# Performance work log

Measured on AMD Instinct MI355X. Metric: run time of the kernel, lower is better.

The kernel has to match this reference:

```python
import jax, jax.numpy as jnp
import numpy as np

N_NODES = 50000
N_EDGES = 800000
NUM_FEATURES = 256
HIDDEN = 256
EMBED = 128


def gcn_conv(x, edge_index, W, b, n_nodes):
    """PyG GCNConv: add self-loops, symmetric normalization, linear (no bias),
    scatter-add aggregation to destination nodes, then add bias."""
    loop = jnp.arange(n_nodes, dtype=edge_index.dtype)
    src = jnp.concatenate([edge_index[0], loop])  # [E + N]
    dst = jnp.concatenate([edge_index[1], loop])  # [E + N]
    # degree of destination nodes (edge weight = 1, self-loop weight = 1)
    deg = jax.ops.segment_sum(jnp.ones_like(src, dtype=x.dtype), dst,
                              num_segments=n_nodes)
    dis = jnp.where(deg > 0, jax.lax.rsqrt(jnp.maximum(deg, 1.0)), 0.0)
    norm = dis[src] * dis[dst]  # [E + N]
    xw = x @ W  # [N, out] project first (cheaper gather when out <= in)
    msg = xw[src] * norm[:, None]  # [E + N, out]
    out = jax.ops.segment_sum(msg, dst, num_segments=n_nodes)
    return out + b


def setup_inputs() -> dict:
    key = jax.random.key(0)
    k1, k2, k3, k4 = jax.random.split(key, 4)
    x = jax.random.normal(k1, (N_NODES, NUM_FEATURES), dtype=jnp.float32)
    edge_index = jax.random.randint(k2, (2, N_EDGES), 0, N_NODES, dtype=jnp.int32)
    W1 = jax.random.normal(k3, (NUM_FEATURES, HIDDEN), dtype=jnp.float32) / np.sqrt(NUM_FEATURES)
    b1 = jnp.zeros((HIDDEN,), dtype=jnp.float32)
    W2 = jax.random.normal(k4, (HIDDEN, EMBED), dtype=jnp.float32) / np.sqrt(HIDDEN)
    b2 = jnp.zeros((EMBED,), dtype=jnp.float32)
    return {"x": x, "edge_index": edge_index, "W1": W1, "b1": b1, "W2": W2, "b2": b2}


def reference(x, edge_index, W1, b1, W2, b2):
    n = x.shape[0]
    h = jax.nn.relu(gcn_conv(x, edge_index, W1, b1, n))
    return gcn_conv(h, edge_index, W2, b2, n)
```

## Files before the change

### kernel.cpp

```cpp
#include <hip/hip_runtime.h>
#include <hip/hip_bf16.h>

#define K_DIM 256

typedef __attribute__((ext_vector_type(8))) short short8;
typedef __attribute__((ext_vector_type(4))) float f32x4;


__global__ void degree_hist_kernel(const int* __restrict__ dst, int E,
                                   int* __restrict__ cnt) {
    int e = blockIdx.x * blockDim.x + threadIdx.x;
    if (e < E) atomicAdd(&cnt[dst[e]], 1);
}

constexpr int SCAN_C = 512;

__global__ __launch_bounds__(256) void scan_phase1(const int* __restrict__ cnt,
                                                   int* __restrict__ bsum, int N) {
    const int t = threadIdx.x;
    const int i0 = blockIdx.x * SCAN_C + 2 * t;
    int s = 0;
    if (i0 < N) s += cnt[i0];
    if (i0 + 1 < N) s += cnt[i0 + 1];
    __shared__ int sh[256];
    sh[t] = s;
    __syncthreads();
    for (int off = 128; off > 0; off >>= 1) {
        if (t < off) sh[t] += sh[t + off];
        __syncthreads();
    }
    if (t == 0) bsum[blockIdx.x] = sh[0];
}

__global__ __launch_bounds__(256) void scan_phase2(int* __restrict__ bsum, int nb,
                                                   int* __restrict__ row_ptr, int N) {
    const int t = threadIdx.x;
    int v = (t < nb) ? bsum[t] : 0;
    __shared__ int sh[256];
    sh[t] = v;
    __syncthreads();
    for (int off = 1; off < 256; off <<= 1) {
        int u = (t >= off) ? sh[t - off] : 0;
        __syncthreads();
        sh[t] += u;
        __syncthreads();
    }
    if (t < nb) bsum[t] = (t == 0) ? 0 : sh[t - 1];
    if (t == 255) row_ptr[N] = sh[255];
}

__global__ __launch_bounds__(256) void scan_phase3(const int* __restrict__ cnt,
                                                   const int* __restrict__ bsum,
                                                   int* __restrict__ row_ptr,
                                                   int* __restrict__ fill,
                                                   float* __restrict__ dis, int N) {
    const int t = threadIdx.x;
    const int i0 = blockIdx.x * SCAN_C + 2 * t;
    const int c0 = (i0 < N) ? cnt[i0] : 0;
    const int c1 = (i0 + 1 < N) ? cnt[i0 + 1] : 0;
    __shared__ int sh[256];
    sh[t] = c0 + c1;
    __syncthreads();
    for (int off = 1; off < 256; off <<= 1) {
        int u = (t >= off) ? sh[t - off] : 0;
        __syncthreads();
        sh[t] += u;
        __syncthreads();
    }
    const int excl = ((t == 0) ? 0 : sh[t - 1]) + bsum[blockIdx.x];
    if (i0 < N) {
        row_ptr[i0] = excl;
        fill[i0] = excl;
        dis[i0] = rsqrtf((float)(c0 + 1));
    }
    if (i0 + 1 < N) {
        row_ptr[i0 + 1] = excl + c0;
        fill[i0 + 1] = excl + c0;
        dis[i0 + 1] = rsqrtf((float)(c1 + 1));
    }
}

__global__ void build_csr_kernel(const int* __restrict__ src,
                                 const int* __restrict__ dst, int E,
                                 int* __restrict__ fill, int* __restrict__ col,
                                 const float* __restrict__ dis,
                                 float* __restrict__ wnorm) {
    int e = blockIdx.x * blockDim.x + threadIdx.x;
    if (e < E) {
        int s = src[e];
        int d = dst[e];
        int pos = atomicAdd(&fill[d], 1);
        col[pos] = s;
        wnorm[pos] = dis[s] * dis[d];
    }
}


__device__ __forceinline__ unsigned short bf16_hi(float v) {
    __hip_bfloat16 h = __float2bfloat16(v);
    return *(unsigned short*)&h;
}
__device__ __forceinline__ float bf16_back(unsigned short u) {
    __hip_bfloat16 h = *(__hip_bfloat16*)&u;
    return __bfloat162float(h);
}
__device__ __forceinline__ float bf2f(unsigned short u) {
    unsigned int b = ((unsigned int)u) << 16;
    float f;
    __builtin_memcpy(&f, &b, 4);
    return f;
}


template <int NCOLS>
__global__ __launch_bounds__(256) void gemm_mfma_kernel(const float* __restrict__ A,
                                                        const float* __restrict__ B,
                                                        unsigned short* __restrict__ C,
                                                        int M) {
    __shared__ unsigned short As_hi[128][40];
    __shared__ unsigned short As_lo[128][40];
    __shared__ unsigned short Bs_hi[128][40];
    __shared__ unsigned short Bs_lo[128][40];

    const int t = threadIdx.x;
    const int lane = t & 63;
    const int wid = t >> 6;
    const int wm = wid >> 1;
    const int wn = wid & 1;
    const int m0 = blockIdx.y * 128;
    const int n0 = blockIdx.x * 128;

    f32x4 acc[4][4];
#pragma unroll
    for (int i = 0; i < 4; ++i)
#pragma unroll
        for (int j = 0; j < 4; ++j) acc[i][j] = (f32x4)(0.f);

    const int a_r = t >> 3;
    const int a_c4 = t & 7;
    const int b_col = t & 127;
    const int b_kq0 = t >> 7;

    for (int k0 = 0; k0 < K_DIM; k0 += 32) {
        __syncthreads();

#pragma unroll
        for (int p = 0; p < 4; ++p) {
            const int row = a_r + p * 32;
            const int grow = min(m0 + row, M - 1);
            const float4 v = *(const float4*)(A + (size_t)grow * K_DIM + k0 + a_c4 * 4);
            unsigned short h0 = bf16_hi(v.x), h1 = bf16_hi(v.y),
                           h2 = bf16_hi(v.z), h3 = bf16_hi(v.w);
            unsigned short l0 = bf16_hi(v.x - bf16_back(h0)),
                           l1 = bf16_hi(v.y - bf16_back(h1)),
                           l2 = bf16_hi(v.z - bf16_back(h2)),
                           l3 = bf16_hi(v.w - bf16_back(h3));
            *(ushort4*)&As_hi[row][a_c4 * 4] = make_ushort4(h0, h1, h2, h3);
            *(ushort4*)&As_lo[row][a_c4 * 4] = make_ushort4(l0, l1, l2, l3);
        }

#pragma unroll
        for (int p = 0; p < 4; ++p) {
            const int kq = b_kq0 + p * 2;
            float v0 = B[(size_t)(k0 + kq * 4 + 0) * NCOLS + n0 + b_col];
            float v1 = B[(size_t)(k0 + kq * 4 + 1) * NCOLS + n0 + b_col];
            float v2 = B[(size_t)(k0 + kq * 4 + 2) * NCOLS + n0 + b_col];
            float v3 = B[(size_t)(k0 + kq * 4 + 3) * NCOLS + n0 + b_col];
            unsigned short h0 = bf16_hi(v0), h1 = bf16_hi(v1),
                           h2 = bf16_hi(v2), h3 = bf16_hi(v3);
            unsigned short l0 = bf16_hi(v0 - bf16_back(h0)),
                           l1 = bf16_hi(v1 - bf16_back(h1)),
                           l2 = bf16_hi(v2 - bf16_back(h2)),
                           l3 = bf16_hi(v3 - bf16_back(h3));
            *(ushort4*)&Bs_hi[b_col][kq * 4] = make_ushort4(h0, h1, h2, h3);
            *(ushort4*)&Bs_lo[b_col][kq * 4] = make_ushort4(l0, l1, l2, l3);
        }

        __syncthreads();

        const int fr = lane & 15;
        const int fk = (lane >> 4) * 8;
        short8 a_hi[4], a_lo[4], b_hi[4], b_lo[4];
#pragma unroll
        for (int fm = 0; fm < 4; ++fm) {
            const int r = wm * 64 + fm * 16 + fr;
            a_hi[fm] = *(const short8*)&As_hi[r][fk];
            a_lo[fm] = *(const short8*)&As_lo[r][fk];
        }
#pragma unroll
        for (int fn = 0; fn < 4; ++fn) {
            const int c = wn * 64 + fn * 16 + fr;
            b_hi[fn] = *(const short8*)&Bs_hi[c][fk];
            b_lo[fn] = *(const short8*)&Bs_lo[c][fk];
        }

#pragma unroll
        for (int fm = 0; fm < 4; ++fm)
#pragma unroll
            for (int fn = 0; fn < 4; ++fn) {
                acc[fm][fn] = __builtin_amdgcn_mfma_f32_16x16x32_bf16(
                    a_hi[fm], b_hi[fn], acc[fm][fn], 0, 0, 0);
                acc[fm][fn] = __builtin_amdgcn_mfma_f32_16x16x32_bf16(
                    a_hi[fm], b_lo[fn], acc[fm][fn], 0, 0, 0);
                acc[fm][fn] = __builtin_amdgcn_mfma_f32_16x16x32_bf16(
                    a_lo[fm], b_hi[fn], acc[fm][fn], 0, 0, 0);
            }
    }

    const int c_col = n0 + wn * 64 + (lane & 15);
    const int r_base = m0 + wm * 64 + (lane >> 4) * 4;
#pragma unroll
    for (int fm = 0; fm < 4; ++fm)
#pragma unroll
        for (int fn = 0; fn < 4; ++fn)
#pragma unroll
            for (int r = 0; r < 4; ++r) {
                const int row = r_base + fm * 16 + r;
                if (row < M)
                    C[(size_t)row * NCOLS + c_col + fn * 16] = bf16_hi(acc[fm][fn][r]);
            }
}


template <int F, bool RELU>
__global__ __launch_bounds__(256) void aggregate_kernel(
    const unsigned short* __restrict__ xw, const int* __restrict__ row_ptr,
    const int* __restrict__ col, const float* __restrict__ wnorm,
    const float* __restrict__ dis, const float* __restrict__ bias,
    float* __restrict__ out, int N) {
    constexpr int VEC = F / 64;
    const int wid = threadIdx.x >> 6;
    const int lane = threadIdx.x & 63;
    const int n = blockIdx.x * 4 + wid;
    if (n >= N) return;

    const float dn = dis[n];
    float acc[VEC];
    {
        const float w = dn * dn;
        const unsigned short* xn = xw + (size_t)n * F + lane * VEC;
        if (VEC == 4) {
            const ushort4 u = *(const ushort4*)xn;
            acc[0] = bf2f(u.x) * w;
            acc[1] = bf2f(u.y) * w;
            acc[2] = bf2f(u.z) * w;
            acc[3] = bf2f(u.w) * w;
        } else {
            const ushort2 u = *(const ushort2*)xn;
            acc[0] = bf2f(u.x) * w;
            acc[1] = bf2f(u.y) * w;
        }
    }

    const int e0 = row_ptr[n];
    const int e1 = row_ptr[n + 1];
    int e = e0;
    for (; e + 2 <= e1; e += 2) {
        const int s0 = col[e];
        const int s1 = col[e + 1];
        const float w0 = wnorm[e];
        const float w1 = wnorm[e + 1];
        const unsigned short* x0 = xw + (size_t)s0 * F + lane * VEC;
        const unsigned short* x1 = xw + (size_t)s1 * F + lane * VEC;
        if (VEC == 4) {
            const ushort4 u0 = *(const ushort4*)x0;
            const ushort4 u1 = *(const ushort4*)x1;
            acc[0] += bf2f(u0.x) * w0 + bf2f(u1.x) * w1;
            acc[1] += bf2f(u0.y) * w0 + bf2f(u1.y) * w1;
            acc[2] += bf2f(u0.z) * w0 + bf2f(u1.z) * w1;
            acc[3] += bf2f(u0.w) * w0 + bf2f(u1.w) * w1;
        } else {
            const ushort2 u0 = *(const ushort2*)x0;
            const ushort2 u1 = *(const ushort2*)x1;
            acc[0] += bf2f(u0.x) * w0 + bf2f(u1.x) * w1;
            acc[1] += bf2f(u0.y) * w0 + bf2f(u1.y) * w1;
        }
    }
    if (e < e1) {
        const int s0 = col[e];
        const float w0 = wnorm[e];
        const unsigned short* x0 = xw + (size_t)s0 * F + lane * VEC;
        if (VEC == 4) {
            const ushort4 u0 = *(const ushort4*)x0;
            acc[0] += bf2f(u0.x) * w0;
            acc[1] += bf2f(u0.y) * w0;
            acc[2] += bf2f(u0.z) * w0;
            acc[3] += bf2f(u0.w) * w0;
        } else {
            const ushort2 u0 = *(const ushort2*)x0;
            acc[0] += bf2f(u0.x) * w0;
            acc[1] += bf2f(u0.y) * w0;
        }
    }

    float* o = out + (size_t)n * F + lane * VEC;
#pragma unroll
    for (int v = 0; v < VEC; ++v) {
        float r = acc[v] + bias[lane * VEC + v];
        if (RELU) r = fmaxf(r, 0.f);
        o[v] = r;
    }
}


extern "C" void kernel_launch(void* const* d_in, const int* in_sizes, int n_in,
                              void* d_out, int out_size, void* d_ws, size_t ws_size,
                              hipStream_t stream) {
    const float* x = (const float*)d_in[0];
    const int* edge = (const int*)d_in[1];
    const float* W1 = (const float*)d_in[2];
    const float* b1 = (const float*)d_in[3];
    const float* W2 = (const float*)d_in[4];
    const float* b2 = (const float*)d_in[5];

    const int N = in_sizes[0] / 256;
    const int E = in_sizes[1] / 2;
    const int* src = edge;
    const int* dst = edge + E;

    char* w = (char*)d_ws;
    auto carve = [&](size_t bytes) {
        char* p = w;
        w += (bytes + 255) & ~(size_t)255;
        return p;
    };
    const int nscan = (N + SCAN_C - 1) / SCAN_C;
    int* cnt = (int*)carve((size_t)N * 4);
    int* row_ptr = (int*)carve((size_t)(N + 1) * 4);
    int* fill = (int*)carve((size_t)N * 4);
    int* col = (int*)carve((size_t)E * 4);
    float* wnorm = (float*)carve((size_t)E * 4);
    float* dis = (float*)carve((size_t)N * 4);
    int* bsum = (int*)carve((size_t)nscan * 4);
    unsigned short* xw1 = (unsigned short*)carve((size_t)N * 256 * 2);
    float* h = (float*)carve((size_t)N * 256 * 4);
    unsigned short* xw2 = xw1;

    float* out = (float*)d_out;

    hipMemsetAsync(cnt, 0, (size_t)N * 4, stream);

    const int eblocks = (E + 255) / 256;
    degree_hist_kernel<<<eblocks, 256, 0, stream>>>(dst, E, cnt);
    scan_phase1<<<nscan, 256, 0, stream>>>(cnt, bsum, N);
    scan_phase2<<<1, 256, 0, stream>>>(bsum, nscan, row_ptr, N);
    scan_phase3<<<nscan, 256, 0, stream>>>(cnt, bsum, row_ptr, fill, dis, N);
    build_csr_kernel<<<eblocks, 256, 0, stream>>>(src, dst, E, fill, col, dis, wnorm);

    {
        dim3 grid(256 / 128, (N + 127) / 128);
        gemm_mfma_kernel<256><<<grid, 256, 0, stream>>>(x, W1, xw1, N);
    }
    aggregate_kernel<256, true><<<(N + 3) / 4, 256, 0, stream>>>(
        xw1, row_ptr, col, wnorm, dis, b1, h, N);

    {
        dim3 grid(128 / 128, (N + 127) / 128);
        gemm_mfma_kernel<128><<<grid, 256, 0, stream>>>(h, W2, xw2, N);
    }
    aggregate_kernel<128, false><<<(N + 3) / 4, 256, 0, stream>>>(
        xw2, row_ptr, col, wnorm, dis, b2, out, N);
}
```

Measured before the change: 366.0 us.

## Fuse whole GCN pipeline into one cooperative persistent kernel with grid syncs

Replaces the sequence of about ten kernel launches (memset, degree histogram, three scan phases, CSR build, two GEMMs, two aggregations) with a single cooperative kernel of 768 persistent blocks that separates the stages with grid.sync(). The aim is to remove per-launch overhead and idle gaps between small kernels. In exchange, every phase now runs on a fixed grid with grid-stride loops, the GEMM and aggregation phases are limited by the occupancy of the fused kernel, and the scan phases leave most blocks idle. If the cooperative launch fails, the code falls back to the original multi-kernel path.

```diff
diff --git a/kernel.cpp b/kernel.cpp
--- a/kernel.cpp
+++ b/kernel.cpp
@@ -1,10 +1,345 @@
 #include <hip/hip_runtime.h>
 #include <hip/hip_bf16.h>
+#include <hip/hip_cooperative_groups.h>
+
+namespace cg = cooperative_groups;
 
 #define K_DIM 256
+constexpr int GRIDN = 768;
+constexpr int BLK = 256;
+constexpr int SCAN_C = 512;
 
 typedef __attribute__((ext_vector_type(8))) short short8;
 typedef __attribute__((ext_vector_type(4))) float f32x4;
+
+
+__device__ __forceinline__ unsigned short bf16_hi(float v) {
+    __hip_bfloat16 h = __float2bfloat16(v);
+    return *(unsigned short*)&h;
+}
+__device__ __forceinline__ float bf16_back(unsigned short u) {
+    __hip_bfloat16 h = *(__hip_bfloat16*)&u;
+    return __bfloat162float(h);
+}
+__device__ __forceinline__ float bf2f(unsigned short u) {
+    unsigned int b = ((unsigned int)u) << 16;
+    float f;
+    __builtin_memcpy(&f, &b, 4);
+    return f;
+}
+
+
+struct Params {
+    const float* x;
+    const int* src;
+    const int* dst;
+    const float* W1;
+    const float* b1;
+    const float* W2;
+    const float* b2;
+    int N, E, nscan;
+    int* cnt;
+    int* row_ptr;
+    int* fill;
+    int* col;
+    int* bsum;
+    float* wnorm;
+    float* dis;
+    float* h;
+    unsigned short* xw1;
+    unsigned short* xw2;
+    float* out;
+};
+
+template <int NCOLS>
+__device__ void gemm_phase(const float* __restrict__ A, const float* __restrict__ B,
+                           unsigned short* __restrict__ C, int M,
+                           unsigned short* lds) {
+    unsigned short(*As_hi)[40] = (unsigned short(*)[40])(lds);
+    unsigned short(*As_lo)[40] = (unsigned short(*)[40])(lds + 128 * 40);
+    unsigned short(*Bs_hi)[40] = (unsigned short(*)[40])(lds + 2 * 128 * 40);
+    unsigned short(*Bs_lo)[40] = (unsigned short(*)[40])(lds + 3 * 128 * 40);
+
+    const int t = threadIdx.x;
+    const int lane = t & 63;
+    const int wid = t >> 6;
+    const int wm = wid >> 1;
+    const int wn = wid & 1;
+
+    const int a_r = t >> 3;
+    const int a_c4 = t & 7;
+    const int b_col = t & 127;
+    const int b_kq0 = t >> 7;
+
+    const int ntn = NCOLS / 128;
+    const int ntm = (M + 127) / 128;
+    const int ntiles = ntm * ntn;
+
+    for (int tile = blockIdx.x; tile < ntiles; tile += GRIDN) {
+        const int m0 = (tile / ntn) * 128;
+        const int n0 = (tile % ntn) * 128;
+
+        f32x4 acc[4][4];
+#pragma unroll
+        for (int i = 0; i < 4; ++i)
+#pragma unroll
+            for (int j = 0; j < 4; ++j) acc[i][j] = (f32x4)(0.f);
+
+        for (int k0 = 0; k0 < K_DIM; k0 += 32) {
+            __syncthreads();
+
+#pragma unroll
+            for (int p = 0; p < 4; ++p) {
+                const int row = a_r + p * 32;
+                const int grow = min(m0 + row, M - 1);
+                const float4 v = *(const float4*)(A + (size_t)grow * K_DIM + k0 + a_c4 * 4);
+                unsigned short h0 = bf16_hi(v.x), h1 = bf16_hi(v.y),
+                               h2 = bf16_hi(v.z), h3 = bf16_hi(v.w);
+                unsigned short l0 = bf16_hi(v.x - bf16_back(h0)),
+                               l1 = bf16_hi(v.y - bf16_back(h1)),
+                               l2 = bf16_hi(v.z - bf16_back(h2)),
+                               l3 = bf16_hi(v.w - bf16_back(h3));
+                *(ushort4*)&As_hi[row][a_c4 * 4] = make_ushort4(h0, h1, h2, h3);
+                *(ushort4*)&As_lo[row][a_c4 * 4] = make_ushort4(l0, l1, l2, l3);
+            }
+
+#pragma unroll
+            for (int p = 0; p < 4; ++p) {
+                const int kq = b_kq0 + p * 2;
+                float v0 = B[(size_t)(k0 + kq * 4 + 0) * NCOLS + n0 + b_col];
+                float v1 = B[(size_t)(k0 + kq * 4 + 1) * NCOLS + n0 + b_col];
+                float v2 = B[(size_t)(k0 + kq * 4 + 2) * NCOLS + n0 + b_col];
+                float v3 = B[(size_t)(k0 + kq * 4 + 3) * NCOLS + n0 + b_col];
+                unsigned short h0 = bf16_hi(v0), h1 = bf16_hi(v1),
+                               h2 = bf16_hi(v2), h3 = bf16_hi(v3);
+                unsigned short l0 = bf16_hi(v0 - bf16_back(h0)),
+                               l1 = bf16_hi(v1 - bf16_back(h1)),
+                               l2 = bf16_hi(v2 - bf16_back(h2)),
+                               l3 = bf16_hi(v3 - bf16_back(h3));
+                *(ushort4*)&Bs_hi[b_col][kq * 4] = make_ushort4(h0, h1, h2, h3);
+                *(ushort4*)&Bs_lo[b_col][kq * 4] = make_ushort4(l0, l1, l2, l3);
+            }
+
+            __syncthreads();
+
+            const int fr = lane & 15;
+            const int fk = (lane >> 4) * 8;
+            short8 a_hi[4], a_lo[4], b_hi[4], b_lo[4];
+#pragma unroll
+            for (int fm = 0; fm < 4; ++fm) {
+                const int r = wm * 64 + fm * 16 + fr;
+                a_hi[fm] = *(const short8*)&As_hi[r][fk];
+                a_lo[fm] = *(const short8*)&As_lo[r][fk];
+            }
+#pragma unroll
+            for (int fn = 0; fn < 4; ++fn) {
+                const int c = wn * 64 + fn * 16 + fr;
+                b_hi[fn] = *(const short8*)&Bs_hi[c][fk];
+                b_lo[fn] = *(const short8*)&Bs_lo[c][fk];
+            }
+
+#pragma unroll
+            for (int fm = 0; fm < 4; ++fm)
+#pragma unroll
+                for (int fn = 0; fn < 4; ++fn) {
+                    acc[fm][fn] = __builtin_amdgcn_mfma_f32_16x16x32_bf16(
+                        a_hi[fm], b_hi[fn], acc[fm][fn], 0, 0, 0);
+                    acc[fm][fn] = __builtin_amdgcn_mfma_f32_16x16x32_bf16(
+                        a_hi[fm], b_lo[fn], acc[fm][fn], 0, 0, 0);
+                    acc[fm][fn] = __builtin_amdgcn_mfma_f32_16x16x32_bf16(
+                        a_lo[fm], b_hi[fn], acc[fm][fn], 0, 0, 0);
+                }
+        }
+
+        const int c_col = n0 + wn * 64 + (lane & 15);
+        const int r_base = m0 + wm * 64 + (lane >> 4) * 4;
+#pragma unroll
+        for (int fm = 0; fm < 4; ++fm)
+#pragma unroll
+            for (int fn = 0; fn < 4; ++fn)
+#pragma unroll
+                for (int r = 0; r < 4; ++r) {
+                    const int row = r_base + fm * 16 + r;
+                    if (row < M)
+                        C[(size_t)row * NCOLS + c_col + fn * 16] = bf16_hi(acc[fm][fn][r]);
+                }
+    }
+}
+
+template <int F, bool RELU>
+__device__ void agg_phase(const unsigned short* __restrict__ xw,
+                          const int* __restrict__ row_ptr, const int* __restrict__ col,
+                          const float* __restrict__ wnorm, const float* __restrict__ dis,
+                          const float* __restrict__ bias, float* __restrict__ out, int N) {
+    constexpr int VEC = F / 64;
+    const int wid = threadIdx.x >> 6;
+    const int lane = threadIdx.x & 63;
+
+    for (int n = blockIdx.x * 4 + wid; n < N; n += GRIDN * 4) {
+        const float dn = dis[n];
+        float acc[VEC];
+        {
+            const float w = dn * dn;
+            const unsigned short* xn = xw + (size_t)n * F + lane * VEC;
+            if (VEC == 4) {
+                const ushort4 u = *(const ushort4*)xn;
+                acc[0] = bf2f(u.x) * w;
+                acc[1] = bf2f(u.y) * w;
+                acc[2] = bf2f(u.z) * w;
+                acc[3] = bf2f(u.w) * w;
+            } else {
+                const ushort2 u = *(const ushort2*)xn;
+                acc[0] = bf2f(u.x) * w;
+                acc[1] = bf2f(u.y) * w;
+            }
+        }
+
+        const int e0 = row_ptr[n];
+        const int e1 = row_ptr[n + 1];
+        int e = e0;
+        for (; e + 4 <= e1; e += 4) {
+            const int s0 = col[e], s1 = col[e + 1], s2 = col[e + 2], s3 = col[e + 3];
+            const float w0 = wnorm[e], w1 = wnorm[e + 1], w2 = wnorm[e + 2], w3 = wnorm[e + 3];
+            const unsigned short* x0 = xw + (size_t)s0 * F + lane * VEC;
+            const unsigned short* x1 = xw + (size_t)s1 * F + lane * VEC;
+            const unsigned short* x2 = xw + (size_t)s2 * F + lane * VEC;
+            const unsigned short* x3 = xw + (size_t)s3 * F + lane * VEC;
+            if (VEC == 4) {
+                const ushort4 u0 = *(const ushort4*)x0;
+                const ushort4 u1 = *(const ushort4*)x1;
+                const ushort4 u2 = *(const ushort4*)x2;
+                const ushort4 u3 = *(const ushort4*)x3;
+                acc[0] += bf2f(u0.x) * w0 + bf2f(u1.x) * w1 + bf2f(u2.x) * w2 + bf2f(u3.x) * w3;
+                acc[1] += bf2f(u0.y) * w0 + bf2f(u1.y) * w1 + bf2f(u2.y) * w2 + bf2f(u3.y) * w3;
+                acc[2] += bf2f(u0.z) * w0 + bf2f(u1.z) * w1 + bf2f(u2.z) * w2 + bf2f(u3.z) * w3;
+                acc[3] += bf2f(u0.w) * w0 + bf2f(u1.w) * w1 + bf2f(u2.w) * w2 + bf2f(u3.w) * w3;
+            } else {
+                const ushort2 u0 = *(const ushort2*)x0;
+                const ushort2 u1 = *(const ushort2*)x1;
+                const ushort2 u2 = *(const ushort2*)x2;
+                const ushort2 u3 = *(const ushort2*)x3;
+                acc[0] += bf2f(u0.x) * w0 + bf2f(u1.x) * w1 + bf2f(u2.x) * w2 + bf2f(u3.x) * w3;
+                acc[1] += bf2f(u0.y) * w0 + bf2f(u1.y) * w1 + bf2f(u2.y) * w2 + bf2f(u3.y) * w3;
+            }
+        }
+        for (; e < e1; ++e) {
+            const int s0 = col[e];
+            const float w0 = wnorm[e];
+            const unsigned short* x0 = xw + (size_t)s0 * F + lane * VEC;
+            if (VEC == 4) {
+                const ushort4 u0 = *(const ushort4*)x0;
+                acc[0] += bf2f(u0.x) * w0;
+                acc[1] += bf2f(u0.y) * w0;
+                acc[2] += bf2f(u0.z) * w0;
+                acc[3] += bf2f(u0.w) * w0;
+            } else {
+                const ushort2 u0 = *(const ushort2*)x0;
+                acc[0] += bf2f(u0.x) * w0;
+                acc[1] += bf2f(u0.y) * w0;
+            }
+        }
+
+        float* o = out + (size_t)n * F + lane * VEC;
+#pragma unroll
+        for (int v = 0; v < VEC; ++v) {
+            float r = acc[v] + bias[lane * VEC + v];
+            if (RELU) r = fmaxf(r, 0.f);
+            o[v] = r;
+        }
+    }
+}
+
+__global__ void __launch_bounds__(256, 3) fused_kernel(Params p) {
+    __shared__ unsigned short lds[4 * 128 * 40];
+    cg::grid_group grid = cg::this_grid();
+    const int t = threadIdx.x;
+    const int bid = blockIdx.x;
+    const int gtid = bid * BLK + t;
+    const int gsize = GRIDN * BLK;
+    int* sh = (int*)lds;
+
+    for (int i = gtid; i < p.N; i += gsize) p.cnt[i] = 0;
+    grid.sync();
+
+    for (int e = gtid; e < p.E; e += gsize) atomicAdd(&p.cnt[p.dst[e]], 1);
+    grid.sync();
+
+    if (bid < p.nscan) {
+        const int i0 = bid * SCAN_C + 2 * t;
+        int s = 0;
+        if (i0 < p.N) s += p.cnt[i0];
+        if (i0 + 1 < p.N) s += p.cnt[i0 + 1];
+        sh[t] = s;
+        __syncthreads();
+        for (int off = 128; off > 0; off >>= 1) {
+            if (t < off) sh[t] += sh[t + off];
+            __syncthreads();
+        }
+        if (t == 0) p.bsum[bid] = sh[0];
+    }
+    grid.sync();
+
+    if (bid == 0) {
+        int v = (t < p.nscan) ? p.bsum[t] : 0;
+        sh[t] = v;
+        __syncthreads();
+        for (int off = 1; off < 256; off <<= 1) {
+            int u = (t >= off) ? sh[t - off] : 0;
+            __syncthreads();
+            sh[t] += u;
+            __syncthreads();
+        }
+        if (t < p.nscan) p.bsum[t] = (t == 0) ? 0 : sh[t - 1];
+        if (t == 255) p.row_ptr[p.N] = sh[255];
+    }
+    grid.sync();
+
+    if (bid < p.nscan) {
+        const int i0 = bid * SCAN_C + 2 * t;
+        const int c0 = (i0 < p.N) ? p.cnt[i0] : 0;
+        const int c1 = (i0 + 1 < p.N) ? p.cnt[i0 + 1] : 0;
+        sh[t] = c0 + c1;
+        __syncthreads();
+        for (int off = 1; off < 256; off <<= 1) {
+            int u = (t >= off) ? sh[t - off] : 0;
+            __syncthreads();
+            sh[t] += u;
+            __syncthreads();
+        }
+        const int excl = ((t == 0) ? 0 : sh[t - 1]) + p.bsum[bid];
+        if (i0 < p.N) {
+            p.row_ptr[i0] = excl;
+            p.fill[i0] = excl;
+            p.dis[i0] = rsqrtf((float)(c0 + 1));
+        }
+        if (i0 + 1 < p.N) {
+            p.row_ptr[i0 + 1] = excl + c0;
+            p.fill[i0 + 1] = excl + c0;
+            p.dis[i0 + 1] = rsqrtf((float)(c1 + 1));
+        }
+    }
+    grid.sync();
+
+    for (int e = gtid; e < p.E; e += gsize) {
+        const int s = p.src[e];
+        const int d = p.dst[e];
+        const int pos = atomicAdd(&p.fill[d], 1);
+        p.col[pos] = s;
+        p.wnorm[pos] = p.dis[s] * p.dis[d];
+    }
+    grid.sync();
+
+    gemm_phase<256>(p.x, p.W1, p.xw1, p.N, lds);
+    grid.sync();
+
+    agg_phase<256, true>(p.xw1, p.row_ptr, p.col, p.wnorm, p.dis, p.b1, p.h, p.N);
+    grid.sync();
+
+    gemm_phase<128>(p.h, p.W2, p.xw2, p.N, lds);
+    grid.sync();
+
+    agg_phase<128, false>(p.xw2, p.row_ptr, p.col, p.wnorm, p.dis, p.b2, p.out, p.N);
+}
 
 
 __global__ void degree_hist_kernel(const int* __restrict__ dst, int E,
@@ -12,8 +347,6 @@
     int e = blockIdx.x * blockDim.x + threadIdx.x;
     if (e < E) atomicAdd(&cnt[dst[e]], 1);
 }
-
-constexpr int SCAN_C = 512;
 
 __global__ __launch_bounds__(256) void scan_phase1(const int* __restrict__ cnt,
                                                    int* __restrict__ bsum, int N) {
@@ -95,55 +428,40 @@
     }
 }
 
-
-__device__ __forceinline__ unsigned short bf16_hi(float v) {
-    __hip_bfloat16 h = __float2bfloat16(v);
-    return *(unsigned short*)&h;
-}
-__device__ __forceinline__ float bf16_back(unsigned short u) {
-    __hip_bfloat16 h = *(__hip_bfloat16*)&u;
-    return __bfloat162float(h);
-}
-__device__ __forceinline__ float bf2f(unsigned short u) {
-    unsigned int b = ((unsigned int)u) << 16;
-    float f;
-    __builtin_memcpy(&f, &b, 4);
-    return f;
-}
-
-
 template <int NCOLS>
 __global__ __launch_bounds__(256) void gemm_mfma_kernel(const float* __restrict__ A,
                                                         const float* __restrict__ B,
                                                         unsigned short* __restrict__ C,
                                                         int M) {
-    __shared__ unsigned short As_hi[128][40];
-    __shared__ unsigned short As_lo[128][40];
-    __shared__ unsigned short Bs_hi[128][40];
-    __shared__ unsigned short Bs_lo[128][40];
-
+    __shared__ unsigned short lds[4 * 128 * 40];
     const int t = threadIdx.x;
+    const int ntn = NCOLS / 128;
+    const int tile = blockIdx.x;
+    unsigned short(*As_hi)[40] = (unsigned short(*)[40])(lds);
+    unsigned short(*As_lo)[40] = (unsigned short(*)[40])(lds + 128 * 40);
+    unsigned short(*Bs_hi)[40] = (unsigned short(*)[40])(lds + 2 * 128 * 40);
+    unsigned short(*Bs_lo)[40] = (unsigned short(*)[40])(lds + 3 * 128 * 40);
+
     const int lane = t & 63;
     const int wid = t >> 6;
     const int wm = wid >> 1;
     const int wn = wid & 1;
-    const int m0 = blockIdx.y * 128;
-    const int n0 = blockIdx.x * 128;
-
-    f32x4 acc[4][4];
-#pragma unroll
-    for (int i = 0; i < 4; ++i)
-#pragma unroll
-        for (int j = 0; j < 4; ++j) acc[i][j] = (f32x4)(0.f);
+    const int m0 = (tile / ntn) * 128;
+    const int n0 = (tile % ntn) * 128;
 
     const int a_r = t >> 3;
     const int a_c4 = t & 7;
     const int b_col = t & 127;
     const int b_kq0 = t >> 7;
 
+    f32x4 acc[4][4];
+#pragma unroll
+    for (int i = 0; i < 4; ++i)
+#pragma unroll
+        for (int j = 0; j < 4; ++j) acc[i][j] = (f32x4)(0.f);
+
     for (int k0 = 0; k0 < K_DIM; k0 += 32) {
         __syncthreads();
-
 #pragma unroll
         for (int p = 0; p < 4; ++p) {
             const int row = a_r + p * 32;
@@ -158,7 +476,6 @@
             *(ushort4*)&As_hi[row][a_c4 * 4] = make_ushort4(h0, h1, h2, h3);
             *(ushort4*)&As_lo[row][a_c4 * 4] = make_ushort4(l0, l1, l2, l3);
         }
-
 #pragma unroll
         for (int p = 0; p < 4; ++p) {
             const int kq = b_kq0 + p * 2;
@@ -175,7 +492,6 @@
             *(ushort4*)&Bs_hi[b_col][kq * 4] = make_ushort4(h0, h1, h2, h3);
             *(ushort4*)&Bs_lo[b_col][kq * 4] = make_ushort4(l0, l1, l2, l3);
         }
-
         __syncthreads();
 
         const int fr = lane & 15;
@@ -193,7 +509,6 @@
             b_hi[fn] = *(const short8*)&Bs_hi[c][fk];
             b_lo[fn] = *(const short8*)&Bs_lo[c][fk];
         }
-
 #pragma unroll
         for (int fm = 0; fm < 4; ++fm)
 #pragma unroll
@@ -220,7 +535,6 @@
                     C[(size_t)row * NCOLS + c_col + fn * 16] = bf16_hi(acc[fm][fn][r]);
             }
 }
-
 
 template <int F, bool RELU>
 __global__ __launch_bounds__(256) void aggregate_kernel(
@@ -338,24 +652,34 @@
 
     float* out = (float*)d_out;
 
+    Params p;
+    p.x = x; p.src = src; p.dst = dst;
+    p.W1 = W1; p.b1 = b1; p.W2 = W2; p.b2 = b2;
+    p.N = N; p.E = E; p.nscan = nscan;
+    p.cnt = cnt; p.row_ptr = row_ptr; p.fill = fill; p.col = col; p.bsum = bsum;
+    p.wnorm = wnorm; p.dis = dis; p.h = h;
+    p.xw1 = xw1; p.xw2 = xw2; p.out = out;
+
+    void* args[] = {(void*)&p};
+    hipError_t err = hipLaunchCooperativeKernel((const void*)fused_kernel,
+                                                dim3(GRIDN), dim3(BLK), args, 0, stream);
+    if (err == hipSuccess) return;
+
     hipMemsetAsync(cnt, 0, (size_t)N * 4, stream);
-
     const int eblocks = (E + 255) / 256;
     degree_hist_kernel<<<eblocks, 256, 0, stream>>>(dst, E, cnt);
     scan_phase1<<<nscan, 256, 0, stream>>>(cnt, bsum, N);
     scan_phase2<<<1, 256, 0, stream>>>(bsum, nscan, row_ptr, N);
     scan_phase3<<<nscan, 256, 0, stream>>>(cnt, bsum, row_ptr, fill, dis, N);
     build_csr_kernel<<<eblocks, 256, 0, stream>>>(src, dst, E, fill, col, dis, wnorm);
-
     {
-        dim3 grid(256 / 128, (N + 127) / 128);
+        dim3 grid(2 * ((N + 127) / 128));
         gemm_mfma_kernel<256><<<grid, 256, 0, stream>>>(x, W1, xw1, N);
     }
     aggregate_kernel<256, true><<<(N + 3) / 4, 256, 0, stream>>>(
         xw1, row_ptr, col, wnorm, dis, b1, h, N);
-
     {
-        dim3 grid(128 / 128, (N + 127) / 128);
+        dim3 grid((N + 127) / 128);
         gemm_mfma_kernel<128><<<grid, 256, 0, stream>>>(h, W2, xw2, N);
     }
     aggregate_kernel<128, false><<<(N + 3) / 4, 256, 0, stream>>>(
```

New measurement: 1.209 ms. +230.2%, slower.

## Fuse CSR construction into one cooperative kernel and unroll aggregation by four

Applied to the files above, without the earlier changes.

Replaces the memset plus five CSR-building launches (degree histogram, three scan phases, fill) with a single cooperative kernel that uses grid-wide syncs between phases, falling back to the old launches if the cooperative launch fails. The aggregation loop now processes four neighbors per iteration to put more gathers in flight. The GEMM grid is flattened to 1D so that column tiles of the same row block are adjacent. The fusion cuts launch overhead and inter-kernel gaps, at the cost of grid-sync latency and a fixed 1024-block grid that serves the grid-stride edge loops.

```diff
diff --git a/kernel.cpp b/kernel.cpp
--- a/kernel.cpp
+++ b/kernel.cpp
@@ -1,10 +1,125 @@
 #include <hip/hip_runtime.h>
 #include <hip/hip_bf16.h>
+#include <hip/hip_cooperative_groups.h>
+
+namespace cg = cooperative_groups;
 
 #define K_DIM 256
+constexpr int BLK = 256;
+constexpr int SCAN_C = 512;
+constexpr int CSR_GRID = 1024;
 
 typedef __attribute__((ext_vector_type(8))) short short8;
 typedef __attribute__((ext_vector_type(4))) float f32x4;
+
+
+__device__ __forceinline__ unsigned short bf16_hi(float v) {
+    __hip_bfloat16 h = __float2bfloat16(v);
+    return *(unsigned short*)&h;
+}
+__device__ __forceinline__ float bf16_back(unsigned short u) {
+    __hip_bfloat16 h = *(__hip_bfloat16*)&u;
+    return __bfloat162float(h);
+}
+__device__ __forceinline__ float bf2f(unsigned short u) {
+    unsigned int b = ((unsigned int)u) << 16;
+    float f;
+    __builtin_memcpy(&f, &b, 4);
+    return f;
+}
+
+
+struct CsrParams {
+    const int* src;
+    const int* dst;
+    int N, E, nscan;
+    int* cnt;
+    int* row_ptr;
+    int* fill;
+    int* col;
+    int* bsum;
+    float* wnorm;
+    float* dis;
+};
+
+__global__ void __launch_bounds__(256, 4) csr_fused_kernel(CsrParams p) {
+    __shared__ int sh[256];
+    cg::grid_group grid = cg::this_grid();
+    const int t = threadIdx.x;
+    const int bid = blockIdx.x;
+    const int gtid = bid * BLK + t;
+    const int gsize = CSR_GRID * BLK;
+
+    for (int i = gtid; i < p.N; i += gsize) p.cnt[i] = 0;
+    grid.sync();
+
+    for (int e = gtid; e < p.E; e += gsize) atomicAdd(&p.cnt[p.dst[e]], 1);
+    grid.sync();
+
+    if (bid < p.nscan) {
+        const int i0 = bid * SCAN_C + 2 * t;
+        int s = 0;
+        if (i0 < p.N) s += p.cnt[i0];
+        if (i0 + 1 < p.N) s += p.cnt[i0 + 1];
+        sh[t] = s;
+        __syncthreads();
+        for (int off = 128; off > 0; off >>= 1) {
+            if (t < off) sh[t] += sh[t + off];
+            __syncthreads();
+        }
+        if (t == 0) p.bsum[bid] = sh[0];
+    }
+    grid.sync();
+
+    if (bid == 0) {
+        int v = (t < p.nscan) ? p.bsum[t] : 0;
+        sh[t] = v;
+        __syncthreads();
+        for (int off = 1; off < 256; off <<= 1) {
+            int u = (t >= off) ? sh[t - off] : 0;
+            __syncthreads();
+            sh[t] += u;
+            __syncthreads();
+        }
+        if (t < p.nscan) p.bsum[t] = (t == 0) ? 0 : sh[t - 1];
+        if (t == 255) p.row_ptr[p.N] = sh[255];
+    }
+    grid.sync();
+
+    if (bid < p.nscan) {
+        const int i0 = bid * SCAN_C + 2 * t;
+        const int c0 = (i0 < p.N) ? p.cnt[i0] : 0;
+        const int c1 = (i0 + 1 < p.N) ? p.cnt[i0 + 1] : 0;
+        sh[t] = c0 + c1;
+        __syncthreads();
+        for (int off = 1; off < 256; off <<= 1) {
+            int u = (t >= off) ? sh[t - off] : 0;
+            __syncthreads();
+            sh[t] += u;
+            __syncthreads();
+        }
+        const int excl = ((t == 0) ? 0 : sh[t - 1]) + p.bsum[bid];
+        if (i0 < p.N) {
+            p.row_ptr[i0] = excl;
+            p.fill[i0] = excl;
+            p.dis[i0] = rsqrtf((float)(c0 + 1));
+        }
+        if (i0 + 1 < p.N) {
+            p.row_ptr[i0 + 1] = excl + c0;
+            p.fill[i0 + 1] = excl + c0;
+            p.dis[i0 + 1] = rsqrtf((float)(c1 + 1));
+        }
+    }
+    grid.sync();
+
+    for (int e = gtid; e < p.E; e += gsize) {
+        const int s = p.src[e];
+        const int d = p.dst[e];
+        const int pos = atomicAdd(&p.fill[d], 1);
+        p.col[pos] = s;
+        p.wnorm[pos] = p.dis[s] * p.dis[d];
+    }
+}
 
 
 __global__ void degree_hist_kernel(const int* __restrict__ dst, int E,
@@ -12,8 +127,6 @@
     int e = blockIdx.x * blockDim.x + threadIdx.x;
     if (e < E) atomicAdd(&cnt[dst[e]], 1);
 }
-
-constexpr int SCAN_C = 512;
 
 __global__ __launch_bounds__(256) void scan_phase1(const int* __restrict__ cnt,
                                                    int* __restrict__ bsum, int N) {
@@ -96,54 +209,40 @@
 }
 
 
-__device__ __forceinline__ unsigned short bf16_hi(float v) {
-    __hip_bfloat16 h = __float2bfloat16(v);
-    return *(unsigned short*)&h;
-}
-__device__ __forceinline__ float bf16_back(unsigned short u) {
-    __hip_bfloat16 h = *(__hip_bfloat16*)&u;
-    return __bfloat162float(h);
-}
-__device__ __forceinline__ float bf2f(unsigned short u) {
-    unsigned int b = ((unsigned int)u) << 16;
-    float f;
-    __builtin_memcpy(&f, &b, 4);
-    return f;
-}
-
-
 template <int NCOLS>
 __global__ __launch_bounds__(256) void gemm_mfma_kernel(const float* __restrict__ A,
                                                         const float* __restrict__ B,
                                                         unsigned short* __restrict__ C,
                                                         int M) {
-    __shared__ unsigned short As_hi[128][40];
-    __shared__ unsigned short As_lo[128][40];
-    __shared__ unsigned short Bs_hi[128][40];
-    __shared__ unsigned short Bs_lo[128][40];
-
+    __shared__ unsigned short lds[4 * 128 * 40];
     const int t = threadIdx.x;
+    const int ntn = NCOLS / 128;
+    const int tile = blockIdx.x;
+    unsigned short(*As_hi)[40] = (unsigned short(*)[40])(lds);
+    unsigned short(*As_lo)[40] = (unsigned short(*)[40])(lds + 128 * 40);
+    unsigned short(*Bs_hi)[40] = (unsigned short(*)[40])(lds + 2 * 128 * 40);
+    unsigned short(*Bs_lo)[40] = (unsigned short(*)[40])(lds + 3 * 128 * 40);
+
     const int lane = t & 63;
     const int wid = t >> 6;
     const int wm = wid >> 1;
     const int wn = wid & 1;
-    const int m0 = blockIdx.y * 128;
-    const int n0 = blockIdx.x * 128;
-
-    f32x4 acc[4][4];
-#pragma unroll
-    for (int i = 0; i < 4; ++i)
-#pragma unroll
-        for (int j = 0; j < 4; ++j) acc[i][j] = (f32x4)(0.f);
+    const int m0 = (tile / ntn) * 128;
+    const int n0 = (tile % ntn) * 128;
 
     const int a_r = t >> 3;
     const int a_c4 = t & 7;
     const int b_col = t & 127;
     const int b_kq0 = t >> 7;
 
+    f32x4 acc[4][4];
+#pragma unroll
+    for (int i = 0; i < 4; ++i)
+#pragma unroll
+        for (int j = 0; j < 4; ++j) acc[i][j] = (f32x4)(0.f);
+
     for (int k0 = 0; k0 < K_DIM; k0 += 32) {
         __syncthreads();
-
 #pragma unroll
         for (int p = 0; p < 4; ++p) {
             const int row = a_r + p * 32;
@@ -158,7 +257,6 @@
             *(ushort4*)&As_hi[row][a_c4 * 4] = make_ushort4(h0, h1, h2, h3);
             *(ushort4*)&As_lo[row][a_c4 * 4] = make_ushort4(l0, l1, l2, l3);
         }
-
 #pragma unroll
         for (int p = 0; p < 4; ++p) {
             const int kq = b_kq0 + p * 2;
@@ -175,7 +273,6 @@
             *(ushort4*)&Bs_hi[b_col][kq * 4] = make_ushort4(h0, h1, h2, h3);
             *(ushort4*)&Bs_lo[b_col][kq * 4] = make_ushort4(l0, l1, l2, l3);
         }
-
         __syncthreads();
 
         const int fr = lane & 15;
@@ -193,7 +290,6 @@
             b_hi[fn] = *(const short8*)&Bs_hi[c][fk];
             b_lo[fn] = *(const short8*)&Bs_lo[c][fk];
         }
-
 #pragma unroll
         for (int fm = 0; fm < 4; ++fm)
 #pragma unroll
@@ -255,28 +351,32 @@
     const int e0 = row_ptr[n];
     const int e1 = row_ptr[n + 1];
     int e = e0;
-    for (; e + 2 <= e1; e += 2) {
-        const int s0 = col[e];
-        const int s1 = col[e + 1];
-        const float w0 = wnorm[e];
-        const float w1 = wnorm[e + 1];
+    for (; e + 4 <= e1; e += 4) {
+        const int s0 = col[e], s1 = col[e + 1], s2 = col[e + 2], s3 = col[e + 3];
+        const float w0 = wnorm[e], w1 = wnorm[e + 1], w2 = wnorm[e + 2], w3 = wnorm[e + 3];
         const unsigned short* x0 = xw + (size_t)s0 * F + lane * VEC;
         const unsigned short* x1 = xw + (size_t)s1 * F + lane * VEC;
+        const unsigned short* x2 = xw + (size_t)s2 * F + lane * VEC;
+        const unsigned short* x3 = xw + (size_t)s3 * F + lane * VEC;
         if (VEC == 4) {
             const ushort4 u0 = *(const ushort4*)x0;
             const ushort4 u1 = *(const ushort4*)x1;
-            acc[0] += bf2f(u0.x) * w0 + bf2f(u1.x) * w1;
-            acc[1] += bf2f(u0.y) * w0 + bf2f(u1.y) * w1;
-            acc[2] += bf2f(u0.z) * w0 + bf2f(u1.z) * w1;
-            acc[3] += bf2f(u0.w) * w0 + bf2f(u1.w) * w1;
+            const ushort4 u2 = *(const ushort4*)x2;
+            const ushort4 u3 = *(const ushort4*)x3;
+            acc[0] += bf2f(u0.x) * w0 + bf2f(u1.x) * w1 + bf2f(u2.x) * w2 + bf2f(u3.x) * w3;
+            acc[1] += bf2f(u0.y) * w0 + bf2f(u1.y) * w1 + bf2f(u2.y) * w2 + bf2f(u3.y) * w3;
+            acc[2] += bf2f(u0.z) * w0 + bf2f(u1.z) * w1 + bf2f(u2.z) * w2 + bf2f(u3.z) * w3;
+            acc[3] += bf2f(u0.w) * w0 + bf2f(u1.w) * w1 + bf2f(u2.w) * w2 + bf2f(u3.w) * w3;
         } else {
             const ushort2 u0 = *(const ushort2*)x0;
             const ushort2 u1 = *(const ushort2*)x1;
-            acc[0] += bf2f(u0.x) * w0 + bf2f(u1.x) * w1;
-            acc[1] += bf2f(u0.y) * w0 + bf2f(u1.y) * w1;
-        }
-    }
-    if (e < e1) {
+            const ushort2 u2 = *(const ushort2*)x2;
+            const ushort2 u3 = *(const ushort2*)x3;
+            acc[0] += bf2f(u0.x) * w0 + bf2f(u1.x) * w1 + bf2f(u2.x) * w2 + bf2f(u3.x) * w3;
+            acc[1] += bf2f(u0.y) * w0 + bf2f(u1.y) * w1 + bf2f(u2.y) * w2 + bf2f(u3.y) * w3;
+        }
+    }
+    for (; e < e1; ++e) {
         const int s0 = col[e];
         const float w0 = wnorm[e];
         const unsigned short* x0 = xw + (size_t)s0 * F + lane * VEC;
@@ -338,24 +438,34 @@
 
     float* out = (float*)d_out;
 
-    hipMemsetAsync(cnt, 0, (size_t)N * 4, stream);
-
-    const int eblocks = (E + 255) / 256;
-    degree_hist_kernel<<<eblocks, 256, 0, stream>>>(dst, E, cnt);
-    scan_phase1<<<nscan, 256, 0, stream>>>(cnt, bsum, N);
-    scan_phase2<<<1, 256, 0, stream>>>(bsum, nscan, row_ptr, N);
-    scan_phase3<<<nscan, 256, 0, stream>>>(cnt, bsum, row_ptr, fill, dis, N);
-    build_csr_kernel<<<eblocks, 256, 0, stream>>>(src, dst, E, fill, col, dis, wnorm);
+    CsrParams cp;
+    cp.src = src; cp.dst = dst;
+    cp.N = N; cp.E = E; cp.nscan = nscan;
+    cp.cnt = cnt; cp.row_ptr = row_ptr; cp.fill = fill; cp.col = col;
+    cp.bsum = bsum; cp.wnorm = wnorm; cp.dis = dis;
+
+    void* args[] = {(void*)&cp};
+    hipError_t err = hipLaunchCooperativeKernel((const void*)csr_fused_kernel,
+                                                dim3(CSR_GRID), dim3(BLK), args, 0, stream);
+    if (err != hipSuccess) {
+        hipMemsetAsync(cnt, 0, (size_t)N * 4, stream);
+        const int eblocks = (E + 255) / 256;
+        degree_hist_kernel<<<eblocks, 256, 0, stream>>>(dst, E, cnt);
+        scan_phase1<<<nscan, 256, 0, stream>>>(cnt, bsum, N);
+        scan_phase2<<<1, 256, 0, stream>>>(bsum, nscan, row_ptr, N);
+        scan_phase3<<<nscan, 256, 0, stream>>>(cnt, bsum, row_ptr, fill, dis, N);
+        build_csr_kernel<<<eblocks, 256, 0, stream>>>(src, dst, E, fill, col, dis, wnorm);
+    }
 
     {
-        dim3 grid(256 / 128, (N + 127) / 128);
+        dim3 grid(2 * ((N + 127) / 128));
         gemm_mfma_kernel<256><<<grid, 256, 0, stream>>>(x, W1, xw1, N);
     }
     aggregate_kernel<256, true><<<(N + 3) / 4, 256, 0, stream>>>(
         xw1, row_ptr, col, wnorm, dis, b1, h, N);
 
     {
-        dim3 grid(128 / 128, (N + 127) / 128);
+        dim3 grid((N + 127) / 128);
         gemm_mfma_kernel<128><<<grid, 256, 0, stream>>>(h, W2, xw2, N);
     }
     aggregate_kernel<128, false><<<(N + 3) / 4, 256, 0, stream>>>(
```

After: 885.3 us. 142% more time.
